# Kernel tuning notes

Measured on AMD Instinct MI355X. Metric: run time of the kernel, lower is better.

The kernel has to match this reference:

```python
import jax, jax.numpy as jnp
import numpy as np

N = 500_000
N_GROUPS = 50_000
D_IN = 64
D_OUT = 64
IN_MLP = D_IN * 3  # x, x - min, x - max (use_num=False)
NEG_SLOPE = 0.2


def setup_inputs() -> dict:
    key = jax.random.key(0)
    k_x, k_c, k_w1, k_w2 = jax.random.split(key, 4)
    x = jax.random.normal(k_x, (N, D_IN), dtype=jnp.float32)
    # CSR pointer: 0 = p0 <= p1 <= ... <= p_{n_groups} = N
    inner = jnp.sort(jax.random.randint(k_c, (N_GROUPS - 1,), 0, N))
    csr_idx = jnp.concatenate([jnp.zeros((1,), jnp.int64 if jax.config.jax_enable_x64 else jnp.int32),
                               inner.astype(jnp.int32),
                               jnp.full((1,), N, jnp.int32)]).astype(jnp.int32)
    # MLP([in_mlp, d_out, d_out], bias=False): two bias-free Linear layers,
    # each followed by LeakyReLU(0.2) (BatchNorm omitted / identity).
    w1 = jax.random.normal(k_w1, (IN_MLP, D_OUT), dtype=jnp.float32) / np.sqrt(IN_MLP)
    w2 = jax.random.normal(k_w2, (D_OUT, D_OUT), dtype=jnp.float32) / np.sqrt(D_OUT)
    return {"x": x, "csr_idx": csr_idx, "w1": w1, "w2": w2}


def _forward(x, csr_idx, w1, w2):
    n = x.shape[0]
    # element -> segment id (jit-safe equivalent of repeat_interleave on lengths)
    seg = jnp.searchsorted(csr_idx, jnp.arange(n, dtype=csr_idx.dtype), side='right') - 1  # [N]
    # segment min/max + gather-back
    seg_min = jax.ops.segment_min(x, seg, num_segments=N_GROUPS)  # [G, D]
    seg_max = jax.ops.segment_max(x, seg, num_segments=N_GROUPS)  # [G, D]
    x_map_min = x - seg_min[seg]
    x_map_max = x - seg_max[seg]
    h = jnp.concatenate([x, x_map_min, x_map_max], axis=1)  # [N, 3*D_IN]
    h = jax.nn.leaky_relu(h @ w1, NEG_SLOPE)
    h = jax.nn.leaky_relu(h @ w2, NEG_SLOPE)
    return h


def reference(x, csr_idx, w1, w2):
    return _forward(x, csr_idx, w1, w2)
```

## Files before the change

### kernel.cpp

```cpp
#include <hip/hip_runtime.h>
#include <math.h>

#define NROWS 500000
#define NGRP  50000
#define NEG   0.2f
#define GPB   16

typedef __attribute__((ext_vector_type(8))) short bf16x8;
typedef __attribute__((ext_vector_type(4))) float f32x4;
typedef unsigned int uint32;

__device__ __forceinline__ float leaky(float h) { return fmaxf(h, NEG * h); }
__device__ __forceinline__ unsigned short f2bf(float v) {
    uint32 u = __float_as_uint(v);
    u += 0x7FFFu + ((u >> 16) & 1u);
    return (unsigned short)(u >> 16);
}
__device__ __forceinline__ float bf2f(unsigned short h) {
    return __uint_as_float((uint32)h << 16);
}
__device__ __forceinline__ uint32 pkbf(float a, float b) {
    uint32 r;
    asm("v_cvt_pk_bf16_f32 %0, %1, %2" : "=v"(r) : "v"(a), "v"(b));
    return r;
}

__global__ void k0_frag(const float* __restrict__ w1, const float* __restrict__ w2,
                        unsigned short* __restrict__ wsf, unsigned short* __restrict__ w2f,
                        unsigned short* __restrict__ wbh, unsigned short* __restrict__ wbl) {
    int r = blockIdx.x * 256 + threadIdx.x;
    if (r >= 8192) return;
    int j = r & 7, q = (r >> 3) & 3, n = (r >> 5) & 63;
    int k = (r >> 11) * 32 + q * 8 + j;
    if (r < 4096) {
        float ws = w1[k * 64 + n] + w1[4096 + k * 64 + n] + w1[8192 + k * 64 + n];
        wsf[r] = f2bf(ws);
        w2f[r] = f2bf(w2[k * 64 + n]);
    }
    float v = w1[(64 + k) * 64 + n];
    unsigned short h = f2bf(v);
    wbh[r] = h;
    wbl[r] = f2bf(v - bf2f(h));
}

__global__ __launch_bounds__(256, 6)
void fused(const float* __restrict__ x, const int* __restrict__ csr,
           const unsigned short* __restrict__ wsf,
           const unsigned short* __restrict__ w2f,
           const unsigned short* __restrict__ wbh,
           const unsigned short* __restrict__ wbl,
           float* __restrict__ out) {
    __shared__ __align__(16) short xb[64 * 72];
    __shared__ __align__(16) short y1s[64 * 72];
    __shared__ float biasL[GPB * 65];
    __shared__ __align__(16) int rowgrpL[64];
    __shared__ int csrl[GPB + 1];

    const int tid = threadIdx.x, w = tid >> 6, lane = tid & 63;
    const int q = lane >> 4, nl = lane & 15;
    const int jb = w * 16;
    const int n = jb + nl;

    const int g0 = blockIdx.x * GPB;
    const int ng = min(GPB, NGRP - g0);
    if (tid <= ng) csrl[tid] = csr[g0 + tid];
    __syncthreads();
    const int p0 = csrl[0], p1 = csrl[ng];

    float* mnF = (float*)y1s;
    {
        const int sub = q;
        const float4* xr = (const float4*)x;

        auto redgrp = [&](int gl, int q0, int cnt,
                          float4 r0, float4 r1, float4 r2, float4 r3) {
            if (cnt <= 0) return;
            float4 mn, mx;
            mn.x = fminf(fminf(r0.x, r1.x), fminf(r2.x, r3.x));
            mn.y = fminf(fminf(r0.y, r1.y), fminf(r2.y, r3.y));
            mn.z = fminf(fminf(r0.z, r1.z), fminf(r2.z, r3.z));
            mn.w = fminf(fminf(r0.w, r1.w), fminf(r2.w, r3.w));
            mx.x = fmaxf(fmaxf(r0.x, r1.x), fmaxf(r2.x, r3.x));
            mx.y = fmaxf(fmaxf(r0.y, r1.y), fmaxf(r2.y, r3.y));
            mx.z = fmaxf(fmaxf(r0.z, r1.z), fmaxf(r2.z, r3.z));
            mx.w = fmaxf(fmaxf(r0.w, r1.w), fmaxf(r2.w, r3.w));
            for (int i = 16; i < cnt; i += 16) {
                int ra = q0 + min(i + sub,      cnt - 1);
                int rb = q0 + min(i + sub + 4,  cnt - 1);
                int rc = q0 + min(i + sub + 8,  cnt - 1);
                int rd = q0 + min(i + sub + 12, cnt - 1);
                float4 a = xr[ra * 16 + nl], b = xr[rb * 16 + nl];
                float4 c = xr[rc * 16 + nl], d = xr[rd * 16 + nl];
                mn.x = fminf(mn.x, fminf(fminf(a.x, b.x), fminf(c.x, d.x)));
                mn.y = fminf(mn.y, fminf(fminf(a.y, b.y), fminf(c.y, d.y)));
                mn.z = fminf(mn.z, fminf(fminf(a.z, b.z), fminf(c.z, d.z)));
                mn.w = fminf(mn.w, fminf(fminf(a.w, b.w), fminf(c.w, d.w)));
                mx.x = fmaxf(mx.x, fmaxf(fmaxf(a.x, b.x), fmaxf(c.x, d.x)));
                mx.y = fmaxf(mx.y, fmaxf(fmaxf(a.y, b.y), fmaxf(c.y, d.y)));
                mx.z = fmaxf(mx.z, fmaxf(fmaxf(a.z, b.z), fmaxf(c.z, d.z)));
                mx.w = fmaxf(mx.w, fmaxf(fmaxf(a.w, b.w), fmaxf(c.w, d.w)));
            }
#pragma unroll
            for (int mk = 16; mk <= 32; mk <<= 1) {
                mn.x = fminf(mn.x, __shfl_xor(mn.x, mk));
                mn.y = fminf(mn.y, __shfl_xor(mn.y, mk));
                mn.z = fminf(mn.z, __shfl_xor(mn.z, mk));
                mn.w = fminf(mn.w, __shfl_xor(mn.w, mk));
                mx.x = fmaxf(mx.x, __shfl_xor(mx.x, mk));
                mx.y = fmaxf(mx.y, __shfl_xor(mx.y, mk));
                mx.z = fmaxf(mx.z, __shfl_xor(mx.z, mk));
                mx.w = fmaxf(mx.w, __shfl_xor(mx.w, mk));
            }
            if (sub == 0) {
                *(float4*)&mnF[gl * 132 + nl * 4]      = mn;
                *(float4*)&mnF[gl * 132 + 64 + nl * 4] = mx;
            }
        };

#pragma unroll
        for (int pr = 0; pr < 2; ++pr) {
            const int gA = w + pr * 8, gB = gA + 4;
            int qA = csrl[gA], cA = csrl[gA + 1] - qA;
            int qB = csrl[gB], cB = csrl[gB + 1] - qB;
            const int bA = (cA > 0) ? qA : 0, iA = max(cA - 1, 0);
            const int bB = (cB > 0) ? qB : 0, iB = max(cB - 1, 0);
            float4 a0 = xr[(bA + min(sub,      iA)) * 16 + nl];
            float4 a1 = xr[(bA + min(sub + 4,  iA)) * 16 + nl];
            float4 a2 = xr[(bA + min(sub + 8,  iA)) * 16 + nl];
            float4 a3 = xr[(bA + min(sub + 12, iA)) * 16 + nl];
            float4 b0 = xr[(bB + min(sub,      iB)) * 16 + nl];
            float4 b1 = xr[(bB + min(sub + 4,  iB)) * 16 + nl];
            float4 b2 = xr[(bB + min(sub + 8,  iB)) * 16 + nl];
            float4 b3 = xr[(bB + min(sub + 12, iB)) * 16 + nl];
            redgrp(gA, qA, cA, a0, a1, a2, a3);
            redgrp(gB, qB, cB, b0, b1, b2, b3);
        }
    }
    __syncthreads();

    {
        const bf16x8* bhv = (const bf16x8*)wbh;
        const bf16x8* blv = (const bf16x8*)wbl;
        f32x4 acc = { 0.f, 0.f, 0.f, 0.f };
#pragma unroll
        for (int ks = 0; ks < 4; ++ks) {
            bf16x8 Bh = bhv[(ks * 64 + n) * 4 + q];
            bf16x8 Bl = blv[(ks * 64 + n) * 4 + q];
            const float* ap = &mnF[nl * 132 + ks * 32 + q * 8];
            f32x4 v0 = *(const f32x4*)ap;
            f32x4 v1 = *(const f32x4*)(ap + 4);
            union U { bf16x8 v; uint32 u[4]; } ah, al;
            ah.u[0] = pkbf(v0[0], v0[1]);
            ah.u[1] = pkbf(v0[2], v0[3]);
            ah.u[2] = pkbf(v1[0], v1[1]);
            ah.u[3] = pkbf(v1[2], v1[3]);
            float r0 = v0[0] - __uint_as_float(ah.u[0] << 16);
            float r1 = v0[1] - __uint_as_float(ah.u[0] & 0xffff0000u);
            float r2 = v0[2] - __uint_as_float(ah.u[1] << 16);
            float r3 = v0[3] - __uint_as_float(ah.u[1] & 0xffff0000u);
            float r4 = v1[0] - __uint_as_float(ah.u[2] << 16);
            float r5 = v1[1] - __uint_as_float(ah.u[2] & 0xffff0000u);
            float r6 = v1[2] - __uint_as_float(ah.u[3] << 16);
            float r7 = v1[3] - __uint_as_float(ah.u[3] & 0xffff0000u);
            al.u[0] = pkbf(r0, r1);
            al.u[1] = pkbf(r2, r3);
            al.u[2] = pkbf(r4, r5);
            al.u[3] = pkbf(r6, r7);
            acc = __builtin_amdgcn_mfma_f32_16x16x32_bf16(ah.v, Bh, acc, 0, 0, 0);
            acc = __builtin_amdgcn_mfma_f32_16x16x32_bf16(al.v, Bh, acc, 0, 0, 0);
            acc = __builtin_amdgcn_mfma_f32_16x16x32_bf16(ah.v, Bl, acc, 0, 0, 0);
        }
#pragma unroll
        for (int r = 0; r < 4; ++r)
            biasL[(q * 4 + r) * 65 + n] = -acc[r];
    }

    const bf16x8* wsv = (const bf16x8*)wsf;
    const bf16x8* w2v = (const bf16x8*)w2f;
    bf16x8 B0 = wsv[n * 4 + q];
    bf16x8 B1 = wsv[(64 + n) * 4 + q];
    bf16x8 C0 = w2v[n * 4 + q];
    bf16x8 C1 = w2v[(64 + n) * 4 + q];

    const int nch = (p1 - p0 + 63) >> 6;
    float4 stg[4];
    {
        int availf = min(64, p1 - p0) * 64;
        const float4* x4 = (const float4*)(x + (size_t)p0 * 64);
#pragma unroll
        for (int i = 0; i < 4; ++i) {
            int f = (i * 256 + tid) * 4;
            if (f < availf) stg[i] = x4[f >> 2];
        }
    }
    __syncthreads();

    for (int ch = 0; ch < nch; ++ch) {
        const int r0c  = p0 + (ch << 6);
        const int rows = min(64, p1 - r0c);
        const int availf = rows * 64;

#pragma unroll
        for (int i = 0; i < 4; ++i) {
            int f = (i * 256 + tid) * 4;
            if (f < availf) {
                float4 v = stg[i];
                int r = f >> 6, c = f & 63;
                uint2 p;
                p.x = pkbf(v.x, v.y);
                p.y = pkbf(v.z, v.w);
                *(uint2*)(&xb[r * 72 + c]) = p;
            }
        }
        if (tid < 64) {
            int rs = min(r0c + tid, p1 - 1);
            int lo = 0, hi = ng;
#pragma unroll
            for (int it = 0; it < 5; ++it) {
                int mid = (lo + hi) >> 1;
                bool cb = csrl[mid] <= rs;
                lo = cb ? mid : lo;
                hi = cb ? hi : mid;
            }
            rowgrpL[tid] = lo;
        }
        __syncthreads();

        if (ch + 1 < nch) {
            int r0n = r0c + 64;
            int availn = min(64, p1 - r0n) * 64;
            const float4* x4 = (const float4*)(x + (size_t)r0n * 64);
#pragma unroll
            for (int i = 0; i < 4; ++i) {
                int f = (i * 256 + tid) * 4;
                if (f < availn) stg[i] = x4[f >> 2];
            }
        }

        f32x4 h[4];
#pragma unroll
        for (int mt = 0; mt < 4; ++mt) {
            int rbase = mt * 16 + q * 4;
            int4 grp = *(const int4*)(&rowgrpL[rbase]);
            f32x4 acc;
            acc.x = biasL[grp.x * 65 + n];
            acc.y = biasL[grp.y * 65 + n];
            acc.z = biasL[grp.z * 65 + n];
            acc.w = biasL[grp.w * 65 + n];
            bf16x8 a0 = *(const bf16x8*)(&xb[(mt * 16 + nl) * 72 + q * 8]);
            bf16x8 a1 = *(const bf16x8*)(&xb[(mt * 16 + nl) * 72 + 32 + q * 8]);
            acc = __builtin_amdgcn_mfma_f32_16x16x32_bf16(a0, B0, acc, 0, 0, 0);
            acc = __builtin_amdgcn_mfma_f32_16x16x32_bf16(a1, B1, acc, 0, 0, 0);
            h[mt] = acc;
        }
#pragma unroll
        for (int mt = 0; mt < 4; ++mt) {
            int rbase = mt * 16 + q * 4;
            float h0 = leaky(h[mt][0]);
            float h1 = leaky(h[mt][1]);
            float h2 = leaky(h[mt][2]);
            float h3 = leaky(h[mt][3]);
            uint32 p01 = pkbf(h0, h1);
            uint32 p23 = pkbf(h2, h3);
            y1s[(rbase + 0) * 72 + n] = (short)(p01 & 0xffffu);
            y1s[(rbase + 1) * 72 + n] = (short)(p01 >> 16);
            y1s[(rbase + 2) * 72 + n] = (short)(p23 & 0xffffu);
            y1s[(rbase + 3) * 72 + n] = (short)(p23 >> 16);
        }
        __syncthreads();

#pragma unroll
        for (int mt = 0; mt < 4; ++mt) {
            f32x4 acc = {0.f, 0.f, 0.f, 0.f};
            bf16x8 a0 = *(const bf16x8*)(&y1s[(mt * 16 + nl) * 72 + q * 8]);
            bf16x8 a1 = *(const bf16x8*)(&y1s[(mt * 16 + nl) * 72 + 32 + q * 8]);
            acc = __builtin_amdgcn_mfma_f32_16x16x32_bf16(a0, C0, acc, 0, 0, 0);
            acc = __builtin_amdgcn_mfma_f32_16x16x32_bf16(a1, C1, acc, 0, 0, 0);
            int rbase = mt * 16 + q * 4;
#pragma unroll
            for (int r = 0; r < 4; ++r) {
                int rl = rbase + r;
                if (rl < rows)
                    out[(size_t)(r0c + rl) * 64 + n] = leaky(acc[r]);
            }
        }
    }
}

extern "C" void kernel_launch(void* const* d_in, const int* in_sizes, int n_in,
                              void* d_out, int out_size, void* d_ws, size_t ws_size,
                              hipStream_t stream) {
    const float* x   = (const float*)d_in[0];
    const int*   csr = (const int*)d_in[1];
    const float* w1  = (const float*)d_in[2];
    const float* w2  = (const float*)d_in[3];
    float* out = (float*)d_out;

    unsigned short* wsf = (unsigned short*)d_ws;
    unsigned short* w2f = wsf + 4096;
    unsigned short* wbh = wsf + 8192;
    unsigned short* wbl = wsf + 16384;

    k0_frag<<<32, 256, 0, stream>>>(w1, w2, wsf, w2f, wbh, wbl);
    const int grid = (NGRP + GPB - 1) / GPB;
    fused<<<grid, 256, 0, stream>>>(x, csr, wsf, w2f, wbh, wbl, out);
}
```

Before: 258.1 us.

## Split fused kernel into group-stat kernel and row-tiled MLP kernel

Splits the single fused kernel into two. The first computes per-group min/max bias terms and a per-row segment id, writing both to global workspace. The second runs the two-layer MLP over fixed 64-row tiles that read the bias from global memory. This removes load imbalance from variable group sizes in the fused kernel, at the cost of reading x twice, an extra launch, and global traffic for the bias and segment arrays.

```diff
diff --git a/kernel.cpp b/kernel.cpp
--- a/kernel.cpp
+++ b/kernel.cpp
@@ -44,30 +44,34 @@
 }
 
 __global__ __launch_bounds__(256, 6)
-void fused(const float* __restrict__ x, const int* __restrict__ csr,
-           const unsigned short* __restrict__ wsf,
-           const unsigned short* __restrict__ w2f,
-           const unsigned short* __restrict__ wbh,
-           const unsigned short* __restrict__ wbl,
-           float* __restrict__ out) {
-    __shared__ __align__(16) short xb[64 * 72];
-    __shared__ __align__(16) short y1s[64 * 72];
-    __shared__ float biasL[GPB * 65];
-    __shared__ __align__(16) int rowgrpL[64];
+void grpstat(const float* __restrict__ x, const int* __restrict__ csr,
+             const unsigned short* __restrict__ wbh,
+             const unsigned short* __restrict__ wbl,
+             float* __restrict__ biasG, int* __restrict__ seg) {
+    __shared__ float mnF[GPB * 132];
     __shared__ int csrl[GPB + 1];
 
     const int tid = threadIdx.x, w = tid >> 6, lane = tid & 63;
     const int q = lane >> 4, nl = lane & 15;
-    const int jb = w * 16;
-    const int n = jb + nl;
+    const int n = w * 16 + nl;
 
     const int g0 = blockIdx.x * GPB;
-    const int ng = min(GPB, NGRP - g0);
-    if (tid <= ng) csrl[tid] = csr[g0 + tid];
-    __syncthreads();
-    const int p0 = csrl[0], p1 = csrl[ng];
-
-    float* mnF = (float*)y1s;
+    if (tid <= GPB) csrl[tid] = csr[g0 + tid];
+    __syncthreads();
+    const int p0 = csrl[0], p1 = csrl[GPB];
+
+    for (int r = p0 + tid; r < p1; r += 256) {
+        int lo = 0, hi = GPB;
+#pragma unroll
+        for (int it = 0; it < 5; ++it) {
+            int mid = (lo + hi) >> 1;
+            bool cb = csrl[mid] <= r;
+            lo = cb ? mid : lo;
+            hi = cb ? hi : mid;
+        }
+        seg[r] = g0 + lo;
+    }
+
     {
         const int sub = q;
         const float4* xr = (const float4*)x;
@@ -172,8 +176,42 @@
         }
 #pragma unroll
         for (int r = 0; r < 4; ++r)
-            biasL[(q * 4 + r) * 65 + n] = -acc[r];
-    }
+            biasG[(size_t)(g0 + q * 4 + r) * 64 + n] = -acc[r];
+    }
+}
+
+__global__ __launch_bounds__(256, 6)
+void mlp(const float* __restrict__ x, const int* __restrict__ seg,
+         const float* __restrict__ biasG,
+         const unsigned short* __restrict__ wsf,
+         const unsigned short* __restrict__ w2f,
+         float* __restrict__ out) {
+    __shared__ __align__(16) short xb[64 * 72];
+    __shared__ __align__(16) short y1s[64 * 72];
+    __shared__ __align__(16) int rowgrpL[64];
+
+    const int tid = threadIdx.x, w = tid >> 6, lane = tid & 63;
+    const int q = lane >> 4, nl = lane & 15;
+    const int n = w * 16 + nl;
+
+    const int r0 = blockIdx.x * 64;
+    const int rows = min(64, NROWS - r0);
+    const int availf = rows * 64;
+
+    const float4* x4 = (const float4*)(x + (size_t)r0 * 64);
+#pragma unroll
+    for (int i = 0; i < 4; ++i) {
+        int f = (i * 256 + tid) * 4;
+        if (f < availf) {
+            float4 v = x4[f >> 2];
+            int r = f >> 6, c = f & 63;
+            uint2 p;
+            p.x = pkbf(v.x, v.y);
+            p.y = pkbf(v.z, v.w);
+            *(uint2*)(&xb[r * 72 + c]) = p;
+        }
+    }
+    if (tid < 64) rowgrpL[tid] = seg[min(r0 + tid, NROWS - 1)];
 
     const bf16x8* wsv = (const bf16x8*)wsf;
     const bf16x8* w2v = (const bf16x8*)w2f;
@@ -181,108 +219,49 @@
     bf16x8 B1 = wsv[(64 + n) * 4 + q];
     bf16x8 C0 = w2v[n * 4 + q];
     bf16x8 C1 = w2v[(64 + n) * 4 + q];
-
-    const int nch = (p1 - p0 + 63) >> 6;
-    float4 stg[4];
-    {
-        int availf = min(64, p1 - p0) * 64;
-        const float4* x4 = (const float4*)(x + (size_t)p0 * 64);
-#pragma unroll
-        for (int i = 0; i < 4; ++i) {
-            int f = (i * 256 + tid) * 4;
-            if (f < availf) stg[i] = x4[f >> 2];
-        }
-    }
-    __syncthreads();
-
-    for (int ch = 0; ch < nch; ++ch) {
-        const int r0c  = p0 + (ch << 6);
-        const int rows = min(64, p1 - r0c);
-        const int availf = rows * 64;
-
-#pragma unroll
-        for (int i = 0; i < 4; ++i) {
-            int f = (i * 256 + tid) * 4;
-            if (f < availf) {
-                float4 v = stg[i];
-                int r = f >> 6, c = f & 63;
-                uint2 p;
-                p.x = pkbf(v.x, v.y);
-                p.y = pkbf(v.z, v.w);
-                *(uint2*)(&xb[r * 72 + c]) = p;
-            }
-        }
-        if (tid < 64) {
-            int rs = min(r0c + tid, p1 - 1);
-            int lo = 0, hi = ng;
-#pragma unroll
-            for (int it = 0; it < 5; ++it) {
-                int mid = (lo + hi) >> 1;
-                bool cb = csrl[mid] <= rs;
-                lo = cb ? mid : lo;
-                hi = cb ? hi : mid;
-            }
-            rowgrpL[tid] = lo;
-        }
-        __syncthreads();
-
-        if (ch + 1 < nch) {
-            int r0n = r0c + 64;
-            int availn = min(64, p1 - r0n) * 64;
-            const float4* x4 = (const float4*)(x + (size_t)r0n * 64);
-#pragma unroll
-            for (int i = 0; i < 4; ++i) {
-                int f = (i * 256 + tid) * 4;
-                if (f < availn) stg[i] = x4[f >> 2];
-            }
-        }
-
-        f32x4 h[4];
-#pragma unroll
-        for (int mt = 0; mt < 4; ++mt) {
-            int rbase = mt * 16 + q * 4;
-            int4 grp = *(const int4*)(&rowgrpL[rbase]);
-            f32x4 acc;
-            acc.x = biasL[grp.x * 65 + n];
-            acc.y = biasL[grp.y * 65 + n];
-            acc.z = biasL[grp.z * 65 + n];
-            acc.w = biasL[grp.w * 65 + n];
-            bf16x8 a0 = *(const bf16x8*)(&xb[(mt * 16 + nl) * 72 + q * 8]);
-            bf16x8 a1 = *(const bf16x8*)(&xb[(mt * 16 + nl) * 72 + 32 + q * 8]);
-            acc = __builtin_amdgcn_mfma_f32_16x16x32_bf16(a0, B0, acc, 0, 0, 0);
-            acc = __builtin_amdgcn_mfma_f32_16x16x32_bf16(a1, B1, acc, 0, 0, 0);
-            h[mt] = acc;
-        }
-#pragma unroll
-        for (int mt = 0; mt < 4; ++mt) {
-            int rbase = mt * 16 + q * 4;
-            float h0 = leaky(h[mt][0]);
-            float h1 = leaky(h[mt][1]);
-            float h2 = leaky(h[mt][2]);
-            float h3 = leaky(h[mt][3]);
-            uint32 p01 = pkbf(h0, h1);
-            uint32 p23 = pkbf(h2, h3);
-            y1s[(rbase + 0) * 72 + n] = (short)(p01 & 0xffffu);
-            y1s[(rbase + 1) * 72 + n] = (short)(p01 >> 16);
-            y1s[(rbase + 2) * 72 + n] = (short)(p23 & 0xffffu);
-            y1s[(rbase + 3) * 72 + n] = (short)(p23 >> 16);
-        }
-        __syncthreads();
-
-#pragma unroll
-        for (int mt = 0; mt < 4; ++mt) {
-            f32x4 acc = {0.f, 0.f, 0.f, 0.f};
-            bf16x8 a0 = *(const bf16x8*)(&y1s[(mt * 16 + nl) * 72 + q * 8]);
-            bf16x8 a1 = *(const bf16x8*)(&y1s[(mt * 16 + nl) * 72 + 32 + q * 8]);
-            acc = __builtin_amdgcn_mfma_f32_16x16x32_bf16(a0, C0, acc, 0, 0, 0);
-            acc = __builtin_amdgcn_mfma_f32_16x16x32_bf16(a1, C1, acc, 0, 0, 0);
-            int rbase = mt * 16 + q * 4;
-#pragma unroll
-            for (int r = 0; r < 4; ++r) {
-                int rl = rbase + r;
-                if (rl < rows)
-                    out[(size_t)(r0c + rl) * 64 + n] = leaky(acc[r]);
-            }
+    __syncthreads();
+
+    f32x4 h[4];
+#pragma unroll
+    for (int mt = 0; mt < 4; ++mt) {
+        int rbase = mt * 16 + q * 4;
+        int4 grp = *(const int4*)(&rowgrpL[rbase]);
+        f32x4 acc;
+        acc.x = biasG[(size_t)grp.x * 64 + n];
+        acc.y = biasG[(size_t)grp.y * 64 + n];
+        acc.z = biasG[(size_t)grp.z * 64 + n];
+        acc.w = biasG[(size_t)grp.w * 64 + n];
+        bf16x8 a0 = *(const bf16x8*)(&xb[(mt * 16 + nl) * 72 + q * 8]);
+        bf16x8 a1 = *(const bf16x8*)(&xb[(mt * 16 + nl) * 72 + 32 + q * 8]);
+        acc = __builtin_amdgcn_mfma_f32_16x16x32_bf16(a0, B0, acc, 0, 0, 0);
+        acc = __builtin_amdgcn_mfma_f32_16x16x32_bf16(a1, B1, acc, 0, 0, 0);
+        h[mt] = acc;
+    }
+#pragma unroll
+    for (int mt = 0; mt < 4; ++mt) {
+        int rbase = mt * 16 + q * 4;
+        uint32 p01 = pkbf(leaky(h[mt][0]), leaky(h[mt][1]));
+        uint32 p23 = pkbf(leaky(h[mt][2]), leaky(h[mt][3]));
+        y1s[(rbase + 0) * 72 + n] = (short)(p01 & 0xffffu);
+        y1s[(rbase + 1) * 72 + n] = (short)(p01 >> 16);
+        y1s[(rbase + 2) * 72 + n] = (short)(p23 & 0xffffu);
+        y1s[(rbase + 3) * 72 + n] = (short)(p23 >> 16);
+    }
+    __syncthreads();
+
+#pragma unroll
+    for (int mt = 0; mt < 4; ++mt) {
+        f32x4 acc = {0.f, 0.f, 0.f, 0.f};
+        bf16x8 a0 = *(const bf16x8*)(&y1s[(mt * 16 + nl) * 72 + q * 8]);
+        bf16x8 a1 = *(const bf16x8*)(&y1s[(mt * 16 + nl) * 72 + 32 + q * 8]);
+        acc = __builtin_amdgcn_mfma_f32_16x16x32_bf16(a0, C0, acc, 0, 0, 0);
+        acc = __builtin_amdgcn_mfma_f32_16x16x32_bf16(a1, C1, acc, 0, 0, 0);
+        int rbase = mt * 16 + q * 4;
+#pragma unroll
+        for (int r = 0; r < 4; ++r) {
+            int rl = rbase + r;
+            if (rl < rows)
+                out[(size_t)(r0 + rl) * 64 + n] = leaky(acc[r]);
         }
     }
 }
@@ -300,8 +279,10 @@
     unsigned short* w2f = wsf + 4096;
     unsigned short* wbh = wsf + 8192;
     unsigned short* wbl = wsf + 16384;
+    float* biasG = (float*)((char*)d_ws + 49152);
+    int*   seg   = (int*)((char*)d_ws + 49152 + 12800000);
 
     k0_frag<<<32, 256, 0, stream>>>(w1, w2, wsf, w2f, wbh, wbl);
-    const int grid = (NGRP + GPB - 1) / GPB;
-    fused<<<grid, 256, 0, stream>>>(x, csr, wsf, w2f, wbh, wbl, out);
-}
+    grpstat<<<NGRP / GPB, 256, 0, stream>>>(x, csr, wbh, wbl, biasG, seg);
+    mlp<<<(NROWS + 63) / 64, 256, 0, stream>>>(x, seg, biasG, wsf, w2f, out);
+}
```

Result: no change. 260.3 us (+0.9%).
